# Optimization experiments

Measured on AMD Instinct MI355X. Metric: run time of the kernel, lower is better.

Reference implementation:

```python
import jax, jax.numpy as jnp
import numpy as np

N_NODES = 100000
N_EDGES = 1600000
K = 5
C = 32
HEADS = 2
LRELU_GAT = 0.2   # SuperGAT negative_slope default
LRELU_OUT = 0.01  # nn.LeakyReLU default
BN_EPS = 1e-5


def setup_inputs() -> dict:
    key = jax.random.key(0)
    ks = jax.random.split(key, 10)
    patch_embs = jax.random.normal(ks[0], (N_NODES, C), dtype=jnp.float32)
    src = jax.random.randint(ks[1], (N_EDGES,), 0, N_NODES, dtype=jnp.int32)
    dst = jax.random.randint(ks[2], (N_EDGES,), 0, N_NODES, dtype=jnp.int32)
    dst = jnp.where(src == dst, (dst + 1) % N_NODES, dst)  # graph has no self-loops
    edge_index = jnp.stack([src, dst])
    edge_attr = jax.random.normal(ks[3], (N_EDGES, 1), dtype=jnp.float32)
    g = 1.0 / np.sqrt(C).astype(np.float32)
    cheb_w = jax.random.normal(ks[4], (K, C, C), dtype=jnp.float32) * g
    cheb_b = jnp.zeros((C,), jnp.float32)
    lin_w = jax.random.normal(ks[5], (C, HEADS * C), dtype=jnp.float32) * g
    att_l = jax.random.normal(ks[6], (HEADS, C), dtype=jnp.float32) * g
    att_r = jax.random.normal(ks[7], (HEADS, C), dtype=jnp.float32) * g
    gat_b = jnp.zeros((C,), jnp.float32)
    bn_g = jnp.ones((C,), jnp.float32)
    bn_b = jnp.zeros((C,), jnp.float32)
    return dict(patch_embs=patch_embs, edge_index=edge_index, edge_attr=edge_attr,
                cheb_w=cheb_w, cheb_b=cheb_b, lin_w=lin_w, att_l=att_l,
                att_r=att_r, gat_b=gat_b, bn_g=bn_g, bn_b=bn_b)


def cheb_conv(x, src, dst, w_edge, cheb_w, cheb_b, n):
    # PyG ChebConv with sym norm, lambda_max=2: L_hat = -D^-1/2 A D^-1/2
    def prop(t):
        return jax.ops.segment_sum(t[src] * w_edge[:, None], dst, num_segments=n)
    Tx0 = x
    out = Tx0 @ cheb_w[0]
    Tx1 = prop(x)
    out = out + Tx1 @ cheb_w[1]
    for k in range(2, cheb_w.shape[0]):
        Tx2 = 2.0 * prop(Tx1) - Tx0
        out = out + Tx2 @ cheb_w[k]
        Tx0, Tx1 = Tx1, Tx2
    return out + cheb_b


def supergat(x, src, dst, lin_w, att_l, att_r, bias, n):
    # SuperGATConv, attention_type='MX', heads=2, concat=False, with self-loops
    H, Ch = att_l.shape
    h = (x @ lin_w).reshape(n, H, Ch)
    xj = h[src]            # [E, H, C] messages from source
    xi = h[dst]            # [E, H, C] target features
    logits = jnp.sum(xi * xj, axis=-1)                         # [E, H]
    alpha = jnp.sum(xj * att_l, -1) + jnp.sum(xi * att_r, -1)  # [E, H]
    alpha = alpha * jax.nn.sigmoid(logits)
    alpha = jax.nn.leaky_relu(alpha, LRELU_GAT)
    # segment softmax over destination nodes
    m = jax.ops.segment_max(alpha, dst, num_segments=n)
    e = jnp.exp(alpha - m[dst])
    s = jax.ops.segment_sum(e, dst, num_segments=n)
    a = e / s[dst]
    out = jax.ops.segment_sum(xj * a[..., None], dst, num_segments=n)  # [N, H, C]
    return out.mean(axis=1) + bias  # concat=False -> head mean


def reference(patch_embs, edge_index, edge_attr, cheb_w, cheb_b, lin_w, att_l,
              att_r, gat_b, bn_g, bn_b):
    n = patch_embs.shape[0]
    src, dst = edge_index[0], edge_index[1]
    # symmetric Laplacian normalization weights
    deg = jax.ops.segment_sum(jnp.ones_like(src, dtype=patch_embs.dtype), src,
                              num_segments=n)
    dis = jnp.where(deg > 0, jax.lax.rsqrt(jnp.maximum(deg, 1.0)), 0.0)
    w_edge = -dis[src] * dis[dst]
    x = cheb_conv(patch_embs, src, dst, w_edge, cheb_w, cheb_b, n)
    # add self-loops for SuperGAT (PyG default add_self_loops=True)
    loop = jnp.arange(n, dtype=src.dtype)
    src2 = jnp.concatenate([src, loop])
    dst2 = jnp.concatenate([dst, loop])
    x2 = supergat(x, src2, dst2, lin_w, att_l, att_r, gat_b, n)
    # LeakyReLU + residual + BatchNorm1d (training-mode batch stats)
    y = jax.nn.leaky_relu(x2, LRELU_OUT) + x2
    mu = y.mean(axis=0)
    var = ((y - mu) ** 2).mean(axis=0)  # biased variance
    return (y - mu) * jax.lax.rsqrt(var + BN_EPS) * bn_g + bn_b
```

## Files before the change

### kernel.cpp

```cpp
#include <hip/hip_runtime.h>
#include <math.h>

#define CC 32
#define CHUNK 4096

static inline int cdiv(long long a, int b) { return (int)((a + b - 1) / b); }

__global__ void k_degcnt(const int* __restrict__ src, const int* __restrict__ dst,
                         float* __restrict__ deg, int* __restrict__ cnt, int E) {
  int e = blockIdx.x * blockDim.x + threadIdx.x;
  if (e < E) {
    atomicAdd(&deg[src[e]], 1.0f);
    atomicAdd(&cnt[dst[e]], 1);
  }
}

__global__ void k_dis(float* __restrict__ dis, int N) {
  int i = blockIdx.x * blockDim.x + threadIdx.x;
  if (i < N) {
    float d = dis[i];
    dis[i] = (d > 0.f) ? rsqrtf(fmaxf(d, 1.f)) : 0.f;
  }
}

__global__ void k_hist(const int* __restrict__ cnt, int* __restrict__ hist, int N) {
  __shared__ int lh[64];
  if (threadIdx.x < 64) lh[threadIdx.x] = 0;
  __syncthreads();
  int i = blockIdx.x * blockDim.x + threadIdx.x;
  if (i < N) atomicAdd(&lh[min(cnt[i], 63)], 1);
  __syncthreads();
  if (threadIdx.x < 64) {
    int v = lh[threadIdx.x];
    if (v) atomicAdd(&hist[threadIdx.x], v);
  }
}

__global__ void k_scanhist(const int* __restrict__ hist, int* __restrict__ hoff) {
  int acc = 0;
  for (int i = 0; i < 64; ++i) { hoff[i] = acc; acc += hist[i]; }
}

__global__ void k_permfill(const int* __restrict__ cnt, int* __restrict__ hoff,
                           int* __restrict__ perm, int N) {
  __shared__ int lh[64], lbase[64];
  if (threadIdx.x < 64) lh[threadIdx.x] = 0;
  __syncthreads();
  int i = blockIdx.x * blockDim.x + threadIdx.x;
  int bin = 0, rank = 0;
  bool act = (i < N);
  if (act) {
    bin = min(cnt[i], 63);
    rank = atomicAdd(&lh[bin], 1);
  }
  __syncthreads();
  if (threadIdx.x < 64) {
    int v = lh[threadIdx.x];
    lbase[threadIdx.x] = v ? atomicAdd(&hoff[threadIdx.x], v) : 0;
  }
  __syncthreads();
  if (act) perm[lbase[bin] + rank] = i;
}

__global__ void k_chunksum(const int* __restrict__ cnt, int* __restrict__ csum, int N) {
  int base = blockIdx.x * CHUNK;
  int v = 0;
  for (int i = threadIdx.x; i < CHUNK; i += 256) {
    int idx = base + i;
    if (idx < N) v += cnt[idx];
  }
  for (int m = 32; m; m >>= 1) v += __shfl_xor(v, m);
  __shared__ int ws[4];
  if ((threadIdx.x & 63) == 0) ws[threadIdx.x >> 6] = v;
  __syncthreads();
  if (threadIdx.x == 0) csum[blockIdx.x] = ws[0] + ws[1] + ws[2] + ws[3];
}

__global__ void k_scancsum(int* __restrict__ csum, int nb, int* __restrict__ rptr,
                           int N, int tot) {
  int acc = 0;
  for (int i = 0; i < nb; ++i) { int v = csum[i]; csum[i] = acc; acc += v; }
  rptr[N] = tot;
}

__global__ void k_fillrptr(int* __restrict__ cnt, const int* __restrict__ csum,
                           int* __restrict__ rptr, int N) {
  int base = blockIdx.x * CHUNK + threadIdx.x * 16;
  int v[16];
  int tot = 0;
#pragma unroll
  for (int q = 0; q < 16; ++q) {
    int idx = base + q;
    v[q] = (idx < N) ? cnt[idx] : 0;
    tot += v[q];
  }
  __shared__ int sh[256];
  sh[threadIdx.x] = tot;
  __syncthreads();
  for (int off = 1; off < 256; off <<= 1) {
    int add = (threadIdx.x >= off) ? sh[threadIdx.x - off] : 0;
    __syncthreads();
    sh[threadIdx.x] += add;
    __syncthreads();
  }
  int excl = sh[threadIdx.x] - tot + csum[blockIdx.x];
#pragma unroll
  for (int q = 0; q < 16; ++q) {
    int idx = base + q;
    if (idx < N) { rptr[idx] = excl; cnt[idx] = excl; }
    excl += v[q];
  }
}

__global__ void k_fill(const int* __restrict__ src, const int* __restrict__ dst,
                       const float* __restrict__ dis, int* __restrict__ cursor,
                       int* __restrict__ gsrc, float* __restrict__ gw, int E) {
  int e = blockIdx.x * blockDim.x + threadIdx.x;
  if (e >= E) return;
  int s = src[e], d = dst[e];
  int p = atomicAdd(&cursor[d], 1);
  gsrc[p] = s;
  gw[p] = -dis[s] * dis[d];
}

__global__ void k_cheb4(const float4* __restrict__ x_in4,
                        const float4* __restrict__ x_sub4,
                        const int* __restrict__ rptr, const int* __restrict__ gsrc,
                        const float* __restrict__ gw, const float* __restrict__ W,
                        const int* __restrict__ perm, float scale,
                        float4* __restrict__ tx_out4, float4* __restrict__ out4,
                        int N) {
  __shared__ float wl[1024];
  for (int i = threadIdx.x; i < 1024; i += 256) wl[i] = W[i];
  __syncthreads();
  int gid = blockIdx.x * 32 + (threadIdx.x >> 3);
  int lane = threadIdx.x & 7;
  if (gid >= N) return;
  int node = perm[gid];
  int beg = rptr[node], end = rptr[node + 1];
  float tx = 0.f, ty = 0.f, tz = 0.f, tw = 0.f;
  for (int base = beg; base < end; base += 8) {
    int rem = end - base;
    int sj = 0; float wjv = 0.f;
    if (lane < rem) { sj = gsrc[base + lane]; wjv = gw[base + lane]; }
    if (rem >= 8) {
#pragma unroll
      for (int q = 0; q < 8; ++q) {
        int s = __shfl(sj, q, 8);
        float w = __shfl(wjv, q, 8);
        float4 j4 = x_in4[(long long)s * 8 + lane];
        tx += w * j4.x; ty += w * j4.y; tz += w * j4.z; tw += w * j4.w;
      }
    } else {
      for (int q = 0; q < rem; ++q) {
        int s = __shfl(sj, q, 8);
        float w = __shfl(wjv, q, 8);
        float4 j4 = x_in4[(long long)s * 8 + lane];
        tx += w * j4.x; ty += w * j4.y; tz += w * j4.z; tw += w * j4.w;
      }
    }
  }
  long long o = (long long)node * 8 + lane;
  float ta[4] = {scale * tx, scale * ty, scale * tz, scale * tw};
  if (x_sub4) {
    float4 s4 = x_sub4[o];
    ta[0] -= s4.x; ta[1] -= s4.y; ta[2] -= s4.z; ta[3] -= s4.w;
  }
  if (tx_out4) {
    float4 t4 = {ta[0], ta[1], ta[2], ta[3]};
    tx_out4[o] = t4;
  }
  float4 a4 = out4[o];
  float ax = 0.f, ay = 0.f, az = 0.f, aw = 0.f;
#pragma unroll
  for (int c = 0; c < 32; ++c) {
    float bc = __shfl(ta[c & 3], c >> 2, 8);
    const float4 w4 = *(const float4*)&wl[c * 32 + lane * 4];
    ax += bc * w4.x; ay += bc * w4.y; az += bc * w4.z; aw += bc * w4.w;
  }
  a4.x += ax; a4.y += ay; a4.z += az; a4.w += aw;
  out4[o] = a4;
}

__global__ void k_gemm32b(const float* __restrict__ T, const float* __restrict__ W,
                          const float* __restrict__ bias, float* __restrict__ out,
                          int N) {
  __shared__ float w[1024];
  for (int i = threadIdx.x; i < 1024; i += 256) w[i] = W[i];
  __syncthreads();
  int row = blockIdx.x * 8 + (threadIdx.x >> 5);
  int col = threadIdx.x & 31;
  if (row >= N) return;
  const float* tr = T + (long long)row * 32;
  float acc = 0.f;
#pragma unroll
  for (int c = 0; c < 32; ++c) acc += tr[c] * w[c * 32 + col];
  out[(long long)row * 32 + col] = acc + bias[col];
}

__global__ void k_gemmh(const float* __restrict__ T, const float* __restrict__ W,
                        const float* __restrict__ attl, const float* __restrict__ attr,
                        float* __restrict__ h, float* __restrict__ bl,
                        float* __restrict__ br, int N) {
  __shared__ float w[2048];
  for (int i = threadIdx.x; i < 2048; i += 256) w[i] = W[i];
  __syncthreads();
  int row = blockIdx.x * 4 + (threadIdx.x >> 6);
  int col = threadIdx.x & 63;
  if (row >= N) return;
  const float* tr = T + (long long)row * 32;
  float acc = 0.f;
#pragma unroll
  for (int c = 0; c < 32; ++c) acc += tr[c] * w[c * 64 + col];
  int ch = col & 31, hd = col >> 5;
  h[(long long)row * 64 + (ch & 15) * 4 + (ch >> 4) + 2 * hd] = acc;
  float pl = acc * attl[col], pr = acc * attr[col];
#pragma unroll
  for (int m = 16; m; m >>= 1) {
    pl += __shfl_xor(pl, m, 64);
    pr += __shfl_xor(pr, m, 64);
  }
  if ((col & 31) == 0) {
    bl[row * 2 + (col >> 5)] = pl;
    br[row * 2 + (col >> 5)] = pr;
  }
}

__device__ inline void gat_edge(const float4& j4, const float4& i4, bool hiH,
                                float bxq, float byq, float brh,
                                float& s0, float& s1, float4& v) {
  float d0 = j4.x * i4.x + j4.y * i4.y;
  float d1 = j4.z * i4.z + j4.w * i4.w;
  d0 += __shfl_xor(d0, 8, 16);
  d1 += __shfl_xor(d1, 8, 16);
  float dc = hiH ? d1 : d0;
  dc += __shfl_xor(dc, 4, 16);
  dc += __shfl_xor(dc, 2, 16);
  dc += __shfl_xor(dc, 1, 16);
  float lin = (hiH ? byq : bxq) + brh;
  float a = lin / (1.f + __expf(-dc));
  a = (a > 0.f) ? a : 0.2f * a;
  float ec = __expf(a);
  float e0 = __shfl(ec, 0, 16), e1 = __shfl(ec, 8, 16);
  s0 += e0; s1 += e1;
  v.x += e0 * j4.x; v.y += e0 * j4.y; v.z += e1 * j4.z; v.w += e1 * j4.w;
}

__global__ void k_expgat4(const float4* __restrict__ h4, const int* __restrict__ rptr,
                          const int* __restrict__ gsrc, const float2* __restrict__ bl,
                          const float2* __restrict__ br, const float* __restrict__ gb,
                          const int* __restrict__ perm, float* __restrict__ y,
                          float* __restrict__ bns, int N) {
  __shared__ float ls[64];
  for (int i = threadIdx.x; i < 64; i += 256) ls[i] = 0.f;
  __syncthreads();
  int gid = blockIdx.x * 16 + (threadIdx.x >> 4);
  int lane = threadIdx.x & 15;
  if (gid < N) {
    int node = perm[gid];
    float4 i4 = h4[(long long)node * 16 + lane];
    float2 brn = br[node], bln = bl[node];
    bool hiH = (lane & 8) != 0;
    float brh = hiH ? brn.y : brn.x;
    float s0 = 0.f, s1 = 0.f;
    float4 v = {0.f, 0.f, 0.f, 0.f};
    gat_edge(i4, i4, hiH, bln.x, bln.y, brh, s0, s1, v);
    int beg = rptr[node], end = rptr[node + 1];
    for (int base = beg; base < end; base += 16) {
      int rem = end - base;
      int sj = 0; float bx = 0.f, by = 0.f;
      if (lane < rem) {
        sj = gsrc[base + lane];
        float2 b2 = bl[sj];
        bx = b2.x; by = b2.y;
      }
      if (rem >= 16) {
#pragma unroll
        for (int p = 0; p < 8; ++p) {
          int qA = p * 2, qB = p * 2 + 1;
          int sA = __shfl(sj, qA, 16);
          int sB = __shfl(sj, qB, 16);
          float4 jA = h4[(long long)sA * 16 + lane];
          float4 jB = h4[(long long)sB * 16 + lane];
          float bxA = __shfl(bx, qA, 16), byA = __shfl(by, qA, 16);
          float bxB = __shfl(bx, qB, 16), byB = __shfl(by, qB, 16);
          gat_edge(jA, i4, hiH, bxA, byA, brh, s0, s1, v);
          gat_edge(jB, i4, hiH, bxB, byB, brh, s0, s1, v);
        }
      } else {
        int q = 0;
        for (; q + 2 <= rem; q += 2) {
          int sA = __shfl(sj, q, 16);
          int sB = __shfl(sj, q + 1, 16);
          float4 jA = h4[(long long)sA * 16 + lane];
          float4 jB = h4[(long long)sB * 16 + lane];
          float bxA = __shfl(bx, q, 16), byA = __shfl(by, q, 16);
          float bxB = __shfl(bx, q + 1, 16), byB = __shfl(by, q + 1, 16);
          gat_edge(jA, i4, hiH, bxA, byA, brh, s0, s1, v);
          gat_edge(jB, i4, hiH, bxB, byB, brh, s0, s1, v);
        }
        if (q < rem) {
          int sA = __shfl(sj, q, 16);
          float4 jA = h4[(long long)sA * 16 + lane];
          float bxA = __shfl(bx, q, 16), byA = __shfl(by, q, 16);
          gat_edge(jA, i4, hiH, bxA, byA, brh, s0, s1, v);
        }
      }
    }
    float x2a = 0.5f * (v.x / s0 + v.z / s1) + gb[lane];
    float x2b = 0.5f * (v.y / s0 + v.w / s1) + gb[lane + 16];
    float ya = ((x2a > 0.f) ? x2a : 0.01f * x2a) + x2a;
    float yb = ((x2b > 0.f) ? x2b : 0.01f * x2b) + x2b;
    y[(long long)node * 32 + lane] = ya;
    y[(long long)node * 32 + lane + 16] = yb;
    atomicAdd(&ls[lane], ya);
    atomicAdd(&ls[lane + 16], yb);
    atomicAdd(&ls[32 + lane], ya * ya);
    atomicAdd(&ls[32 + lane + 16], yb * yb);
  }
  __syncthreads();
  if (threadIdx.x < 64) atomicAdd(&bns[threadIdx.x], ls[threadIdx.x]);
}

__global__ void k_bnfinal(const float* __restrict__ y, const float* __restrict__ bns,
                          const float* __restrict__ g, const float* __restrict__ b,
                          float* __restrict__ out, int N) {
  int i = blockIdx.x * blockDim.x + threadIdx.x;
  if (i >= N * CC) return;
  int c = i & 31;
  float inv_n = 1.f / (float)N;
  float mu = bns[c] * inv_n;
  float var = bns[32 + c] * inv_n - mu * mu;
  out[i] = (y[i] - mu) * rsqrtf(var + 1e-5f) * g[c] + b[c];
}

extern "C" void kernel_launch(void* const* d_in, const int* in_sizes, int n_in,
                              void* d_out, int out_size, void* d_ws, size_t ws_size,
                              hipStream_t stream) {
  const float* patch = (const float*)d_in[0];
  const int* eidx = (const int*)d_in[1];
  const float* cheb_w = (const float*)d_in[3];
  const float* cheb_b = (const float*)d_in[4];
  const float* lin_w = (const float*)d_in[5];
  const float* att_l = (const float*)d_in[6];
  const float* att_r = (const float*)d_in[7];
  const float* gat_b = (const float*)d_in[8];
  const float* bn_g = (const float*)d_in[9];
  const float* bn_b = (const float*)d_in[10];
  float* out = (float*)d_out;

  const int N = in_sizes[0] / CC;
  const int E = in_sizes[1] / 2;
  const int* src = eidx;
  const int* dst = eidx + E;

  float* R0 = (float*)d_ws;
  float* R1 = R0 + (size_t)N * 32;
  float* gw = R1 + (size_t)N * 32;
  int* gsrc = (int*)(gw + E);
  int* grptr = gsrc + E;
  int* cnt = grptr + (N + 2);
  int* csum = cnt + N;
  int* hist = csum + 64;
  float* dis = (float*)(hist + 64);
  float* bns = dis + N;
  int* hoff = (int*)(bns + 64);
  int* perm = hoff + 64;
  float* bl = (float*)(perm + N);
  float* br = bl + (size_t)N * 2;
  float* h = R0;

  const int B = 256;
  const long long NC = (long long)N * 32;

  hipMemsetAsync(cnt, 0, sizeof(int) * ((size_t)N * 2 + 192), stream);

  k_degcnt<<<cdiv(E, B), B, 0, stream>>>(src, dst, dis, cnt, E);
  k_dis<<<cdiv(N, B), B, 0, stream>>>(dis, N);

  k_hist<<<cdiv(N, 1024), 1024, 0, stream>>>(cnt, hist, N);
  k_scanhist<<<1, 1, 0, stream>>>(hist, hoff);
  k_permfill<<<cdiv(N, 1024), 1024, 0, stream>>>(cnt, hoff, perm, N);

  int nb = cdiv(N, CHUNK);
  k_chunksum<<<nb, B, 0, stream>>>(cnt, csum, N);
  k_scancsum<<<1, 1, 0, stream>>>(csum, nb, grptr, N, E);
  k_fillrptr<<<nb, B, 0, stream>>>(cnt, csum, grptr, N);
  k_fill<<<cdiv(E, B), B, 0, stream>>>(src, dst, dis, cnt, gsrc, gw, E);

  k_gemm32b<<<cdiv(N, 8), B, 0, stream>>>(patch, cheb_w, cheb_b, out, N);
  k_cheb4<<<cdiv(N, 32), B, 0, stream>>>((const float4*)patch, nullptr, grptr, gsrc,
                                         gw, cheb_w + 1024, perm, 1.f,
                                         (float4*)R0, (float4*)out, N);
  k_cheb4<<<cdiv(N, 32), B, 0, stream>>>((const float4*)R0, (const float4*)patch,
                                         grptr, gsrc, gw, cheb_w + 2048, perm, 2.f,
                                         (float4*)R1, (float4*)out, N);
  k_cheb4<<<cdiv(N, 32), B, 0, stream>>>((const float4*)R1, (const float4*)R0,
                                         grptr, gsrc, gw, cheb_w + 3072, perm, 2.f,
                                         (float4*)R0, (float4*)out, N);
  k_cheb4<<<cdiv(N, 32), B, 0, stream>>>((const float4*)R0, (const float4*)R1,
                                         grptr, gsrc, gw, cheb_w + 4096, perm, 2.f,
                                         nullptr, (float4*)out, N);

  k_gemmh<<<cdiv(N, 4), B, 0, stream>>>(out, lin_w, att_l, att_r, h, bl, br, N);
  k_expgat4<<<cdiv(N, 16), B, 0, stream>>>((const float4*)h, grptr, gsrc,
                                           (const float2*)bl, (const float2*)br,
                                           gat_b, perm, out, bns, N);
  k_bnfinal<<<cdiv(NC, B), B, 0, stream>>>(out, bns, bn_g, bn_b, out, N);
}
```

Baseline: 734.0 us.

## Privatize degree counters into replicated arrays and pack edge src/weight pairs

New measurement: 699.6 us. -4.7%, faster.

```diff
diff --git a/kernel.cpp b/kernel.cpp
--- a/kernel.cpp
+++ b/kernel.cpp
@@ -3,50 +3,75 @@
 
 #define CC 32
 #define CHUNK 4096
+#define NCPY 16
+#define REDB 1024
 
 static inline int cdiv(long long a, int b) { return (int)((a + b - 1) / b); }
 
-__global__ void k_degcnt(const int* __restrict__ src, const int* __restrict__ dst,
-                         float* __restrict__ deg, int* __restrict__ cnt, int E) {
+__global__ void k_cnt(const int* __restrict__ src, const int* __restrict__ dst,
+                      int* __restrict__ priv, int E, int N) {
   int e = blockIdx.x * blockDim.x + threadIdx.x;
-  if (e < E) {
-    atomicAdd(&deg[src[e]], 1.0f);
-    atomicAdd(&cnt[dst[e]], 1);
-  }
-}
-
-__global__ void k_dis(float* __restrict__ dis, int N) {
-  int i = blockIdx.x * blockDim.x + threadIdx.x;
-  if (i < N) {
-    float d = dis[i];
-    dis[i] = (d > 0.f) ? rsqrtf(fmaxf(d, 1.f)) : 0.f;
-  }
-}
-
-__global__ void k_hist(const int* __restrict__ cnt, int* __restrict__ hist, int N) {
+  if (e >= E) return;
+  int* p = priv + (size_t)(blockIdx.x & (NCPY - 1)) * N;
+  atomicAdd(&p[src[e]], 1 << 16);
+  atomicAdd(&p[dst[e]], 1);
+}
+
+__global__ void k_reduce(int* __restrict__ priv, float* __restrict__ dis,
+                         int* __restrict__ cnt, int* __restrict__ histmat, int N) {
   __shared__ int lh[64];
   if (threadIdx.x < 64) lh[threadIdx.x] = 0;
   __syncthreads();
-  int i = blockIdx.x * blockDim.x + threadIdx.x;
-  if (i < N) atomicAdd(&lh[min(cnt[i], 63)], 1);
-  __syncthreads();
-  if (threadIdx.x < 64) {
-    int v = lh[threadIdx.x];
-    if (v) atomicAdd(&hist[threadIdx.x], v);
-  }
-}
-
-__global__ void k_scanhist(const int* __restrict__ hist, int* __restrict__ hoff) {
-  int acc = 0;
-  for (int i = 0; i < 64; ++i) { hoff[i] = acc; acc += hist[i]; }
-}
-
-__global__ void k_permfill(const int* __restrict__ cnt, int* __restrict__ hoff,
-                           int* __restrict__ perm, int N) {
+  int n = blockIdx.x * REDB + threadIdx.x;
+  if (n < N) {
+    int vals[NCPY];
+    int tot = 0;
+#pragma unroll
+    for (int c = 0; c < NCPY; ++c) {
+      vals[c] = priv[(size_t)c * N + n];
+      tot += vals[c];
+    }
+    int deg = tot >> 16, cv = tot & 0xFFFF;
+    dis[n] = (deg > 0) ? rsqrtf((float)deg) : 0.f;
+    cnt[n] = cv;
+    int acc = 0;
+#pragma unroll
+    for (int c = 0; c < NCPY; ++c) {
+      priv[(size_t)c * N + n] = acc;
+      acc += vals[c] & 0xFFFF;
+    }
+    atomicAdd(&lh[min(cv, 63)], 1);
+  }
+  __syncthreads();
+  if (threadIdx.x < 64) histmat[blockIdx.x * 64 + threadIdx.x] = lh[threadIdx.x];
+}
+
+__global__ void k_scanhist2(int* __restrict__ histmat, int nb) {
+  int lane = threadIdx.x;
+  int tot = 0;
+  for (int i = 0; i < nb; ++i) tot += histmat[i * 64 + lane];
+  __shared__ int sh[64], pf[64];
+  sh[lane] = tot;
+  __syncthreads();
+  if (lane == 0) {
+    int acc = 0;
+    for (int b = 0; b < 64; ++b) { pf[b] = acc; acc += sh[b]; }
+  }
+  __syncthreads();
+  int acc = pf[lane];
+  for (int i = 0; i < nb; ++i) {
+    int v = histmat[i * 64 + lane];
+    histmat[i * 64 + lane] = acc;
+    acc += v;
+  }
+}
+
+__global__ void k_permfill2(const int* __restrict__ cnt, const int* __restrict__ histmat,
+                            int* __restrict__ perm, int N) {
   __shared__ int lh[64], lbase[64];
   if (threadIdx.x < 64) lh[threadIdx.x] = 0;
   __syncthreads();
-  int i = blockIdx.x * blockDim.x + threadIdx.x;
+  int i = blockIdx.x * REDB + threadIdx.x;
   int bin = 0, rank = 0;
   bool act = (i < N);
   if (act) {
@@ -54,10 +79,7 @@
     rank = atomicAdd(&lh[bin], 1);
   }
   __syncthreads();
-  if (threadIdx.x < 64) {
-    int v = lh[threadIdx.x];
-    lbase[threadIdx.x] = v ? atomicAdd(&hoff[threadIdx.x], v) : 0;
-  }
+  if (threadIdx.x < 64) lbase[threadIdx.x] = histmat[blockIdx.x * 64 + threadIdx.x];
   __syncthreads();
   if (act) perm[lbase[bin] + rank] = i;
 }
@@ -107,29 +129,31 @@
 #pragma unroll
   for (int q = 0; q < 16; ++q) {
     int idx = base + q;
-    if (idx < N) { rptr[idx] = excl; cnt[idx] = excl; }
+    if (idx < N) rptr[idx] = excl;
     excl += v[q];
   }
 }
 
-__global__ void k_fill(const int* __restrict__ src, const int* __restrict__ dst,
-                       const float* __restrict__ dis, int* __restrict__ cursor,
-                       int* __restrict__ gsrc, float* __restrict__ gw, int E) {
+__global__ void k_fill3(const int* __restrict__ src, const int* __restrict__ dst,
+                        const float* __restrict__ dis, const int* __restrict__ rptr,
+                        int* __restrict__ priv, int2* __restrict__ eg, int E, int N) {
   int e = blockIdx.x * blockDim.x + threadIdx.x;
   if (e >= E) return;
   int s = src[e], d = dst[e];
-  int p = atomicAdd(&cursor[d], 1);
-  gsrc[p] = s;
-  gw[p] = -dis[s] * dis[d];
+  int* pc = priv + (size_t)(blockIdx.x & (NCPY - 1)) * N;
+  int p = rptr[d] + atomicAdd(&pc[d], 1);
+  int2 v;
+  v.x = s;
+  v.y = __float_as_int(-dis[s] * dis[d]);
+  eg[p] = v;
 }
 
 __global__ void k_cheb4(const float4* __restrict__ x_in4,
                         const float4* __restrict__ x_sub4,
-                        const int* __restrict__ rptr, const int* __restrict__ gsrc,
-                        const float* __restrict__ gw, const float* __restrict__ W,
-                        const int* __restrict__ perm, float scale,
-                        float4* __restrict__ tx_out4, float4* __restrict__ out4,
-                        int N) {
+                        const int* __restrict__ rptr, const int2* __restrict__ eg,
+                        const float* __restrict__ W, const int* __restrict__ perm,
+                        float scale, float4* __restrict__ tx_out4,
+                        float4* __restrict__ out4, int N) {
   __shared__ float wl[1024];
   for (int i = threadIdx.x; i < 1024; i += 256) wl[i] = W[i];
   __syncthreads();
@@ -142,7 +166,11 @@
   for (int base = beg; base < end; base += 8) {
     int rem = end - base;
     int sj = 0; float wjv = 0.f;
-    if (lane < rem) { sj = gsrc[base + lane]; wjv = gw[base + lane]; }
+    if (lane < rem) {
+      int2 v = eg[base + lane];
+      sj = v.x;
+      wjv = __int_as_float(v.y);
+    }
     if (rem >= 8) {
 #pragma unroll
       for (int q = 0; q < 8; ++q) {
@@ -247,7 +275,7 @@
 }
 
 __global__ void k_expgat4(const float4* __restrict__ h4, const int* __restrict__ rptr,
-                          const int* __restrict__ gsrc, const float2* __restrict__ bl,
+                          const int2* __restrict__ eg, const float2* __restrict__ bl,
                           const float2* __restrict__ br, const float* __restrict__ gb,
                           const int* __restrict__ perm, float* __restrict__ y,
                           float* __restrict__ bns, int N) {
@@ -270,7 +298,7 @@
       int rem = end - base;
       int sj = 0; float bx = 0.f, by = 0.f;
       if (lane < rem) {
-        sj = gsrc[base + lane];
+        sj = eg[base + lane].x;
         float2 b2 = bl[sj];
         bx = b2.x; by = b2.y;
       }
@@ -356,54 +384,53 @@
 
   float* R0 = (float*)d_ws;
   float* R1 = R0 + (size_t)N * 32;
-  float* gw = R1 + (size_t)N * 32;
-  int* gsrc = (int*)(gw + E);
-  int* grptr = gsrc + E;
+  int2* eg = (int2*)(R1 + (size_t)N * 32);
+  int* grptr = (int*)(eg + E);
   int* cnt = grptr + (N + 2);
   int* csum = cnt + N;
-  int* hist = csum + 64;
-  float* dis = (float*)(hist + 64);
+  float* dis = (float*)(csum + 64);
   float* bns = dis + N;
-  int* hoff = (int*)(bns + 64);
-  int* perm = hoff + 64;
+  int* perm = (int*)(bns + 64);
   float* bl = (float*)(perm + N);
   float* br = bl + (size_t)N * 2;
+  int* priv = (int*)(br + (size_t)N * 2);
+  int* histmat = priv + (size_t)NCPY * N;
   float* h = R0;
 
   const int B = 256;
   const long long NC = (long long)N * 32;
-
-  hipMemsetAsync(cnt, 0, sizeof(int) * ((size_t)N * 2 + 192), stream);
-
-  k_degcnt<<<cdiv(E, B), B, 0, stream>>>(src, dst, dis, cnt, E);
-  k_dis<<<cdiv(N, B), B, 0, stream>>>(dis, N);
-
-  k_hist<<<cdiv(N, 1024), 1024, 0, stream>>>(cnt, hist, N);
-  k_scanhist<<<1, 1, 0, stream>>>(hist, hoff);
-  k_permfill<<<cdiv(N, 1024), 1024, 0, stream>>>(cnt, hoff, perm, N);
+  int nbred = cdiv(N, REDB);
+
+  hipMemsetAsync(priv, 0, sizeof(int) * (size_t)NCPY * N, stream);
+  hipMemsetAsync(bns, 0, sizeof(float) * 64, stream);
+
+  k_cnt<<<cdiv(E, B), B, 0, stream>>>(src, dst, priv, E, N);
+  k_reduce<<<nbred, REDB, 0, stream>>>(priv, dis, cnt, histmat, N);
+  k_scanhist2<<<1, 64, 0, stream>>>(histmat, nbred);
+  k_permfill2<<<nbred, REDB, 0, stream>>>(cnt, histmat, perm, N);
 
   int nb = cdiv(N, CHUNK);
   k_chunksum<<<nb, B, 0, stream>>>(cnt, csum, N);
   k_scancsum<<<1, 1, 0, stream>>>(csum, nb, grptr, N, E);
   k_fillrptr<<<nb, B, 0, stream>>>(cnt, csum, grptr, N);
-  k_fill<<<cdiv(E, B), B, 0, stream>>>(src, dst, dis, cnt, gsrc, gw, E);
+  k_fill3<<<cdiv(E, B), B, 0, stream>>>(src, dst, dis, grptr, priv, eg, E, N);
 
   k_gemm32b<<<cdiv(N, 8), B, 0, stream>>>(patch, cheb_w, cheb_b, out, N);
-  k_cheb4<<<cdiv(N, 32), B, 0, stream>>>((const float4*)patch, nullptr, grptr, gsrc,
-                                         gw, cheb_w + 1024, perm, 1.f,
+  k_cheb4<<<cdiv(N, 32), B, 0, stream>>>((const float4*)patch, nullptr, grptr, eg,
+                                         cheb_w + 1024, perm, 1.f,
                                          (float4*)R0, (float4*)out, N);
   k_cheb4<<<cdiv(N, 32), B, 0, stream>>>((const float4*)R0, (const float4*)patch,
-                                         grptr, gsrc, gw, cheb_w + 2048, perm, 2.f,
+                                         grptr, eg, cheb_w + 2048, perm, 2.f,
                                          (float4*)R1, (float4*)out, N);
   k_cheb4<<<cdiv(N, 32), B, 0, stream>>>((const float4*)R1, (const float4*)R0,
-                                         grptr, gsrc, gw, cheb_w + 3072, perm, 2.f,
+                                         grptr, eg, cheb_w + 3072, perm, 2.f,
                                          (float4*)R0, (float4*)out, N);
   k_cheb4<<<cdiv(N, 32), B, 0, stream>>>((const float4*)R0, (const float4*)R1,
-                                         grptr, gsrc, gw, cheb_w + 4096, perm, 2.f,
+                                         grptr, eg, cheb_w + 4096, perm, 2.f,
                                          nullptr, (float4*)out, N);
 
   k_gemmh<<<cdiv(N, 4), B, 0, stream>>>(out, lin_w, att_l, att_r, h, bl, br, N);
-  k_expgat4<<<cdiv(N, 16), B, 0, stream>>>((const float4*)h, grptr, gsrc,
+  k_expgat4<<<cdiv(N, 16), B, 0, stream>>>((const float4*)h, grptr, eg,
                                            (const float2*)bl, (const float2*)br,
                                            gat_b, perm, out, bns, N);
   k_bnfinal<<<cdiv(NC, B), B, 0, stream>>>(out, bns, bn_g, bn_b, out, N);
```
